# Kernel tuning notes

Hardware: AMD Instinct MI355X
Metric: run time of the kernel (lower is better)

## Reference

```python
import jax, jax.numpy as jnp
import numpy as np

# J2 (von Mises) plane-strain elastoplasticity with linear isotropic hardening
# (faithful stand-in for pyprnn's J2Material: elastic predictor + radial return,
#  committed history = plastic strain tensor + accumulated plastic strain).
E_MOD = 3130.0   # Young's modulus (epoxy, MPa)
NU = 0.37        # Poisson ratio
SIG_Y = 64.8     # initial yield stress
H_ISO = 300.0    # linear isotropic hardening modulus
MU = E_MOD / (2.0 * (1.0 + NU))
LAM = E_MOD * NU / ((1.0 + NU) * (1.0 - 2.0 * NU))


def j2_update(eps, eps_p, alpha):
    """eps: [P,3] (exx, eyy, gamma_xy engineering); eps_p: [P,4] (xx,yy,zz,xy tensorial);
    alpha: [P] accumulated plastic strain. Returns (stress [P,3], eps_p_new, alpha_new)."""
    ee_xx = eps[:, 0] - eps_p[:, 0]
    ee_yy = eps[:, 1] - eps_p[:, 1]
    ee_zz = -eps_p[:, 2]                      # plane strain: total ezz = 0
    ee_xy = 0.5 * eps[:, 2] - eps_p[:, 3]     # tensorial shear
    tr = ee_xx + ee_yy + ee_zz
    # trial (elastic predictor) stress
    sxx = LAM * tr + 2.0 * MU * ee_xx
    syy = LAM * tr + 2.0 * MU * ee_yy
    szz = LAM * tr + 2.0 * MU * ee_zz
    sxy = 2.0 * MU * ee_xy
    p = (sxx + syy + szz) / 3.0
    dxx, dyy, dzz = sxx - p, syy - p, szz - p
    q = jnp.sqrt(1.5 * (dxx * dxx + dyy * dyy + dzz * dzz + 2.0 * sxy * sxy))
    f = q - (SIG_Y + H_ISO * alpha)
    dgam = jnp.maximum(f, 0.0) / (3.0 * MU + H_ISO)   # radial return, closed form
    qs = jnp.maximum(q, 1e-12)
    nxx, nyy, nzz, nxy = 1.5 * dxx / qs, 1.5 * dyy / qs, 1.5 * dzz / qs, 1.5 * sxy / qs
    two_mu_dg = 2.0 * MU * dgam
    sig = jnp.stack([sxx - two_mu_dg * nxx, syy - two_mu_dg * nyy, sxy - two_mu_dg * nxy], axis=-1)
    eps_p_new = eps_p + dgam[:, None] * jnp.stack([nxx, nyy, nzz, nxy], axis=-1)
    alpha_new = alpha + dgam
    return sig, eps_p_new, alpha_new


def setup_inputs() -> dict:
    key = jax.random.key(0)
    k1, k2, k3 = jax.random.split(key, 3)
    B, T, F = 16384, 128, 3
    MATPTS = 16
    L, O = MATPTS * F, 3
    x = jax.random.normal(k1, (B, T, F), dtype=jnp.float32) * 0.02  # strain paths
    W1 = jax.random.normal(k2, (L, F), dtype=jnp.float32) * (1.0 / np.sqrt(F))
    W2 = jax.random.normal(k3, (O, L), dtype=jnp.float32) * (1.0 / np.sqrt(L))
    return {"x": x, "W1": W1, "W2": W2}


def reference(x, W1, W2):
    B, T, F = x.shape
    L = W1.shape[0]
    P = B * (L // F)                 # total material points = batch * mat_pts
    W2s = jax.nn.softplus(W2)        # SoftLayer: positive weights, no bias
    xt = jnp.swapaxes(x, 0, 1)       # [T, B, F]

    def step(carry, xi):
        eps_p, alpha = carry
        lat = xi @ W1.T                       # fc1 (no bias): [B, L]
        eps = lat.reshape(P, F)               # per-material-point strain
        sig, eps_p, alpha = j2_update(eps, eps_p, alpha)   # update + commit
        out = sig.reshape(B, L) @ W2s.T       # fc2 softplus-weighted linear
        return (eps_p, alpha), out

    carry0 = (jnp.zeros((P, 4), jnp.float32), jnp.zeros((P,), jnp.float32))
    _, ys = jax.lax.scan(step, carry0, xt)    # ys: [T, B, O]
    return jnp.swapaxes(ys, 0, 1)             # [B, T, O]
```

## Files before the change

kernel.cpp:

```cpp
#include <hip/hip_runtime.h>
#include <math.h>


#define BLOCK 256
#define BPB 32
#define TSTEPS 128
#define ROWF (TSTEPS * 3)

typedef float v2 __attribute__((ext_vector_type(2)));

static __device__ __forceinline__ v2 vfma(v2 a, v2 b, v2 c) {
    return __builtin_elementwise_fma(a, b, c);
}
static __device__ __forceinline__ v2 vmax(v2 a, v2 b) {
    return __builtin_elementwise_max(a, b);
}

#define DPP_ADDST(v, ctrl)                                                   \
    v += __int_as_float(__builtin_amdgcn_update_dpp(                         \
        0, __float_as_int(v), (ctrl), 0xf, 0xf, true))
#define RED8(v)                                                              \
    do { DPP_ADDST(v, 0xB1); DPP_ADDST(v, 0x4E); DPP_ADDST(v, 0x141); } while (0)

#define DPP_ST(r, ctrl) "v_add_f32_dpp %" #r ", %" #r ", %" #r " " ctrl \
                        " row_mask:0xf bank_mask:0xf\n\t"
#define DPP_STAGE(ctrl) \
    DPP_ST(0, ctrl) DPP_ST(1, ctrl) DPP_ST(2, ctrl)  DPP_ST(3, ctrl) \
    DPP_ST(4, ctrl) DPP_ST(5, ctrl) DPP_ST(6, ctrl)  DPP_ST(7, ctrl) \
    DPP_ST(8, ctrl) DPP_ST(9, ctrl) DPP_ST(10, ctrl) DPP_ST(11, ctrl)
#define DPP_BFLY12(a0,a1,a2,a3,a4,a5,a6,a7,a8,a9,a10,a11)                    \
  asm volatile(                                                              \
    "s_nop 1\n\t"                                                            \
    DPP_STAGE("quad_perm:[1,0,3,2]")                                         \
    DPP_STAGE("quad_perm:[2,3,0,1]")                                         \
    DPP_STAGE("row_half_mirror")                                             \
    : "+v"(a0), "+v"(a1), "+v"(a2), "+v"(a3), "+v"(a4), "+v"(a5),            \
      "+v"(a6), "+v"(a7), "+v"(a8), "+v"(a9), "+v"(a10), "+v"(a11))

__global__ __launch_bounds__(BLOCK, 2)
void prnn_j2_kernel(const float* __restrict__ x,
                    const float* __restrict__ W1,
                    const float* __restrict__ W2,
                    float* __restrict__ out)
{
    constexpr float MU    = (float)(3130.0 / (2.0 * (1.0 + 0.37)));
    constexpr float LAM   = (float)(3130.0 * 0.37 / ((1.0 + 0.37) * (1.0 - 2.0 * 0.37)));
    constexpr float SIG_Y = 64.8f;
    constexpr float H_ISO = 300.0f;
    const float TWO_MU  = 2.0f * MU;
    const float INV_DEN = 1.0f / (3.0f * MU + H_ISO);
    const float K3P     = (3.0f * MU) * INV_DEN;
    const float HP      = H_ISO * INV_DEN;
    const float CSC     = 1.0f / (MU * 2.4494897427831781f);
    const float Y0      = SIG_Y * CSC;

    const int tid = threadIdx.x;
    const int g   = tid >> 3;
    const int l   = tid & 7;
    const int gb  = blockIdx.x * BPB + g;

    const float* xb = x + gb * ROWF;
    float* ob = out + gb * ROWF;

    const int pa = l, pb = l + 8;
    v2 w1p[3][3], w2p[3][3];
    #pragma unroll
    for (int c = 0; c < 3; ++c)
        #pragma unroll
        for (int f = 0; f < 3; ++f) {
            float s = (c == 2) ? 0.5f : 1.0f;
            w1p[c][f].x = s * W1[(3 * pa + c) * 3 + f];
            w1p[c][f].y = s * W1[(3 * pb + c) * 3 + f];
        }
    #pragma unroll
    for (int o = 0; o < 3; ++o)
        #pragma unroll
        for (int c = 0; c < 3; ++c) {
            float wa = W2[o * 48 + 3 * pa + c];
            float wb = W2[o * 48 + 3 * pb + c];
            w2p[o][c].x = fmaxf(wa, 0.0f) + log1pf(expf(-fabsf(wa)));
            w2p[o][c].y = fmaxf(wb, 0.0f) + log1pf(expf(-fabsf(wb)));
        }

    float Mrow[3];
    {
        float Ms[3][3];
        #pragma unroll
        for (int f = 0; f < 3; ++f) {
            v2 ax = (LAM + TWO_MU) * w1p[0][f] + LAM * w1p[1][f];
            v2 ay = LAM * w1p[0][f] + (LAM + TWO_MU) * w1p[1][f];
            v2 as = TWO_MU * w1p[2][f];
            #pragma unroll
            for (int o = 0; o < 3; ++o) {
                v2 mp = vfma(w2p[o][0], ax, vfma(w2p[o][1], ay, w2p[o][2] * as));
                float ms = mp.x + mp.y;
                RED8(ms);
                Ms[o][f] = ms;
            }
        }
        #pragma unroll
        for (int f = 0; f < 3; ++f) {
            float v = (l == 0) ? Ms[0][f] : ((l == 1) ? Ms[1][f] : Ms[2][f]);
            Mrow[f] = v;
        }
    }

    v2 p0 = {0.f,0.f}, p1 = {0.f,0.f}, p2 = {0.f,0.f}, p3 = {0.f,0.f};
    v2 Y  = {Y0, Y0};
    v2 z0 = {0.f,0.f}, z1 = {0.f,0.f}, z2 = {0.f,0.f};

    const float4* xv = (const float4*)xb;
    const bool wact = (l < 3);
    float* obl = ob + l;

#define J2_PHYS(x0_, x1_, x2_, rr, mxv)                                      \
  {                                                                          \
    const float x0s = (x0_), x1s = (x1_), x2s = (x2_);                       \
    const v2 x0 = {x0s, x0s}, x1 = {x1s, x1s}, x2 = {x2s, x2s};              \
    const v2 wx0 = vfma(w1p[0][0], x0, vfma(w1p[0][1], x1, w1p[0][2] * x2)); \
    const v2 wx1 = vfma(w1p[1][0], x0, vfma(w1p[1][1], x1, w1p[1][2] * x2)); \
    const v2 wxy = vfma(w1p[2][0], x0, vfma(w1p[2][1], x1, w1p[2][2] * x2)); \
    const v2 c3  = (wx0 + wx1) * (1.0f / 3.0f);                              \
    const v2 ex0 = wx0 - c3;                                                 \
    const v2 ey0 = wx1 - c3;                                                 \
    const v2 exd = ex0 - p0;                                                 \
    const v2 eyd = ey0 - p1;                                                 \
    const v2 exy = wxy - p3;                                                 \
    const v2 szd = p2 + c3;                                      \
    const v2 t2 = exy * exy;                                                 \
    const v2 ua = vfma(eyd, eyd, exd * exd);                                 \
    const v2 ub = vfma(t2, (v2){2.0f, 2.0f}, szd * szd);                     \
    v2 u = ua + ub;                                                          \
    u = vmax(u, (v2){1e-30f, 1e-30f});                                       \
    v2 rq;                                                                   \
    rq.x = __builtin_amdgcn_rsqf(u.x);                                       \
    rq.y = __builtin_amdgcn_rsqf(u.y);                                       \
    const v2 su = u * rq;                                       \
    const v2 fY = vmax(su - Y, (v2){0.0f, 0.0f});                            \
    Y = vfma((v2){HP, HP}, fY, Y);                                           \
    const v2 k = (K3P * fY) * rq;                                            \
    const v2 kdx = k * exd;                                                  \
    const v2 kdy = k * eyd;                                                  \
    const v2 kdxy = k * exy;                                                 \
    p0 += kdx;                                                               \
    p1 += kdy;                                                               \
    p3 += kdxy;                                                              \
    p2 = p2 - k * szd;                                                       \
    z0 = vfma(w2p[0][0], kdx, vfma(w2p[0][1], kdy, vfma(w2p[0][2], kdxy, z0)));\
    z1 = vfma(w2p[1][0], kdx, vfma(w2p[1][1], kdy, vfma(w2p[1][2], kdxy, z1)));\
    z2 = vfma(w2p[2][0], kdx, vfma(w2p[2][1], kdy, vfma(w2p[2][2], kdxy, z2)));\
    (rr)[0] = z0.x + z0.y;                                                   \
    (rr)[1] = z1.x + z1.y;                                                   \
    (rr)[2] = z2.x + z2.y;                                                   \
    (mxv) = fmaf(Mrow[0], x0s, fmaf(Mrow[1], x1s, Mrow[2] * x2s));           \
  }

    float4 A0 = xv[0], A1 = xv[1], A2 = xv[2];

    for (int tb = 0; tb < TSTEPS / 4; ++tb) {
        const int nb = (tb < TSTEPS / 4 - 1) ? (3 * tb + 3) : (3 * tb);
        float4 An0 = xv[nb + 0];
        float4 An1 = xv[nb + 1];
        float4 An2 = xv[nb + 2];

        float r[12], mx[4];
        J2_PHYS(A0.x,  A0.y,  A0.z,  r + 0, mx[0]);
        J2_PHYS(A0.w,  A1.x,  A1.y,  r + 3, mx[1]);
        J2_PHYS(A1.z,  A1.w,  A2.x,  r + 6, mx[2]);
        J2_PHYS(A2.y,  A2.z,  A2.w,  r + 9, mx[3]);

        DPP_BFLY12(r[0], r[1], r[2], r[3], r[4], r[5],
                   r[6], r[7], r[8], r[9], r[10], r[11]);

        if (wact) {
            float zz0 = (l == 0) ? r[0] : ((l == 1) ? r[1]  : r[2]);
            float zz1 = (l == 0) ? r[3] : ((l == 1) ? r[4]  : r[5]);
            float zz2 = (l == 0) ? r[6] : ((l == 1) ? r[7]  : r[8]);
            float zz3 = (l == 0) ? r[9] : ((l == 1) ? r[10] : r[11]);
            obl[12 * tb + 0] = fmaf(-TWO_MU, zz0, mx[0]);
            obl[12 * tb + 3] = fmaf(-TWO_MU, zz1, mx[1]);
            obl[12 * tb + 6] = fmaf(-TWO_MU, zz2, mx[2]);
            obl[12 * tb + 9] = fmaf(-TWO_MU, zz3, mx[3]);
        }

        A0 = An0; A1 = An1; A2 = An2;
    }
#undef J2_PHYS
}

extern "C" void kernel_launch(void* const* d_in, const int* in_sizes, int n_in,
                              void* d_out, int out_size, void* d_ws, size_t ws_size,
                              hipStream_t stream) {
    const float* x  = (const float*)d_in[0];
    const float* W1 = (const float*)d_in[1];
    const float* W2 = (const float*)d_in[2];
    float* out = (float*)d_out;

    const int B = 16384;
    dim3 grid(B / BPB);
    dim3 block(BLOCK);
    prnn_j2_kernel<<<grid, block, 0, stream>>>(x, W1, W2, out);
}
```

Measured before the change: 118.7 us.

## Fold deviatoric projection into weights and process eight timesteps per iteration

Precomputes deviatoric-projected and sqrt2-scaled W1 rows so the per-step strain needs fewer ops, drops the separate zz plastic-strain state by using szd = exd+eyd, and rewrites the radial return with a single clamp on 1 - Y*rsqrt(u). It also doubles the time-step batch per loop iteration to 8, with a 24-register DPP butterfly and six float4 prefetches. Together these cut ALU work per step and amortize the reduction and store overhead, at the cost of higher register pressure under the 2-block launch bound.

```diff
diff --git a/kernel.cpp b/kernel.cpp
--- a/kernel.cpp
+++ b/kernel.cpp
@@ -24,18 +24,24 @@
 
 #define DPP_ST(r, ctrl) "v_add_f32_dpp %" #r ", %" #r ", %" #r " " ctrl \
                         " row_mask:0xf bank_mask:0xf\n\t"
-#define DPP_STAGE(ctrl) \
-    DPP_ST(0, ctrl) DPP_ST(1, ctrl) DPP_ST(2, ctrl)  DPP_ST(3, ctrl) \
-    DPP_ST(4, ctrl) DPP_ST(5, ctrl) DPP_ST(6, ctrl)  DPP_ST(7, ctrl) \
-    DPP_ST(8, ctrl) DPP_ST(9, ctrl) DPP_ST(10, ctrl) DPP_ST(11, ctrl)
-#define DPP_BFLY12(a0,a1,a2,a3,a4,a5,a6,a7,a8,a9,a10,a11)                    \
+#define DPP_STAGE24(ctrl) \
+    DPP_ST(0, ctrl)  DPP_ST(1, ctrl)  DPP_ST(2, ctrl)  DPP_ST(3, ctrl)  \
+    DPP_ST(4, ctrl)  DPP_ST(5, ctrl)  DPP_ST(6, ctrl)  DPP_ST(7, ctrl)  \
+    DPP_ST(8, ctrl)  DPP_ST(9, ctrl)  DPP_ST(10, ctrl) DPP_ST(11, ctrl) \
+    DPP_ST(12, ctrl) DPP_ST(13, ctrl) DPP_ST(14, ctrl) DPP_ST(15, ctrl) \
+    DPP_ST(16, ctrl) DPP_ST(17, ctrl) DPP_ST(18, ctrl) DPP_ST(19, ctrl) \
+    DPP_ST(20, ctrl) DPP_ST(21, ctrl) DPP_ST(22, ctrl) DPP_ST(23, ctrl)
+#define DPP_BFLY24(a0,a1,a2,a3,a4,a5,a6,a7,a8,a9,a10,a11,                    \
+                   a12,a13,a14,a15,a16,a17,a18,a19,a20,a21,a22,a23)          \
   asm volatile(                                                              \
     "s_nop 1\n\t"                                                            \
-    DPP_STAGE("quad_perm:[1,0,3,2]")                                         \
-    DPP_STAGE("quad_perm:[2,3,0,1]")                                         \
-    DPP_STAGE("row_half_mirror")                                             \
+    DPP_STAGE24("quad_perm:[1,0,3,2]")                                       \
+    DPP_STAGE24("quad_perm:[2,3,0,1]")                                       \
+    DPP_STAGE24("row_half_mirror")                                           \
     : "+v"(a0), "+v"(a1), "+v"(a2), "+v"(a3), "+v"(a4), "+v"(a5),            \
-      "+v"(a6), "+v"(a7), "+v"(a8), "+v"(a9), "+v"(a10), "+v"(a11))
+      "+v"(a6), "+v"(a7), "+v"(a8), "+v"(a9), "+v"(a10), "+v"(a11),          \
+      "+v"(a12), "+v"(a13), "+v"(a14), "+v"(a15), "+v"(a16), "+v"(a17),      \
+      "+v"(a18), "+v"(a19), "+v"(a20), "+v"(a21), "+v"(a22), "+v"(a23))
 
 __global__ __launch_bounds__(BLOCK, 2)
 void prnn_j2_kernel(const float* __restrict__ x,
@@ -53,6 +59,8 @@
     const float HP      = H_ISO * INV_DEN;
     const float CSC     = 1.0f / (MU * 2.4494897427831781f);
     const float Y0      = SIG_Y * CSC;
+    const float SQRT2   = 1.41421356237309515f;
+    const float RSQRT2  = 0.70710678118654752f;
 
     const int tid = threadIdx.x;
     const int g   = tid >> 3;
@@ -63,15 +71,17 @@
     float* ob = out + gb * ROWF;
 
     const int pa = l, pb = l + 8;
-    v2 w1p[3][3], w2p[3][3];
-    #pragma unroll
-    for (int c = 0; c < 3; ++c)
-        #pragma unroll
-        for (int f = 0; f < 3; ++f) {
-            float s = (c == 2) ? 0.5f : 1.0f;
-            w1p[c][f].x = s * W1[(3 * pa + c) * 3 + f];
-            w1p[c][f].y = s * W1[(3 * pb + c) * 3 + f];
-        }
+    v2 w1r0[3], w1r1[3], w1h2[3];
+    #pragma unroll
+    for (int f = 0; f < 3; ++f) {
+        w1r0[f].x = W1[(3 * pa + 0) * 3 + f];
+        w1r0[f].y = W1[(3 * pb + 0) * 3 + f];
+        w1r1[f].x = W1[(3 * pa + 1) * 3 + f];
+        w1r1[f].y = W1[(3 * pb + 1) * 3 + f];
+        w1h2[f].x = 0.5f * W1[(3 * pa + 2) * 3 + f];
+        w1h2[f].y = 0.5f * W1[(3 * pb + 2) * 3 + f];
+    }
+    v2 w2p[3][3];
     #pragma unroll
     for (int o = 0; o < 3; ++o)
         #pragma unroll
@@ -87,9 +97,9 @@
         float Ms[3][3];
         #pragma unroll
         for (int f = 0; f < 3; ++f) {
-            v2 ax = (LAM + TWO_MU) * w1p[0][f] + LAM * w1p[1][f];
-            v2 ay = LAM * w1p[0][f] + (LAM + TWO_MU) * w1p[1][f];
-            v2 as = TWO_MU * w1p[2][f];
+            v2 ax = (LAM + TWO_MU) * w1r0[f] + LAM * w1r1[f];
+            v2 ay = LAM * w1r0[f] + (LAM + TWO_MU) * w1r1[f];
+            v2 as = TWO_MU * w1h2[f];
             #pragma unroll
             for (int o = 0; o < 3; ++o) {
                 v2 mp = vfma(w2p[o][0], ax, vfma(w2p[o][1], ay, w2p[o][2] * as));
@@ -105,7 +115,17 @@
         }
     }
 
-    v2 p0 = {0.f,0.f}, p1 = {0.f,0.f}, p2 = {0.f,0.f}, p3 = {0.f,0.f};
+    v2 wdx[3], wdy[3], wsh[3];
+    #pragma unroll
+    for (int f = 0; f < 3; ++f) {
+        wdx[f] = (2.0f * w1r0[f] - w1r1[f]) * (1.0f / 3.0f);
+        wdy[f] = (2.0f * w1r1[f] - w1r0[f]) * (1.0f / 3.0f);
+        wsh[f] = SQRT2 * w1h2[f];
+    }
+    #pragma unroll
+    for (int o = 0; o < 3; ++o) w2p[o][2] *= RSQRT2;
+
+    v2 p0 = {0.f,0.f}, p1 = {0.f,0.f}, ps = {0.f,0.f};
     v2 Y  = {Y0, Y0};
     v2 z0 = {0.f,0.f}, z1 = {0.f,0.f}, z2 = {0.f,0.f};
 
@@ -117,38 +137,33 @@
   {                                                                          \
     const float x0s = (x0_), x1s = (x1_), x2s = (x2_);                       \
     const v2 x0 = {x0s, x0s}, x1 = {x1s, x1s}, x2 = {x2s, x2s};              \
-    const v2 wx0 = vfma(w1p[0][0], x0, vfma(w1p[0][1], x1, w1p[0][2] * x2)); \
-    const v2 wx1 = vfma(w1p[1][0], x0, vfma(w1p[1][1], x1, w1p[1][2] * x2)); \
-    const v2 wxy = vfma(w1p[2][0], x0, vfma(w1p[2][1], x1, w1p[2][2] * x2)); \
-    const v2 c3  = (wx0 + wx1) * (1.0f / 3.0f);                              \
-    const v2 ex0 = wx0 - c3;                                                 \
-    const v2 ey0 = wx1 - c3;                                                 \
+    const v2 ex0 = vfma(wdx[0], x0, vfma(wdx[1], x1, wdx[2] * x2));          \
+    const v2 ey0 = vfma(wdy[0], x0, vfma(wdy[1], x1, wdy[2] * x2));          \
+    const v2 wsy = vfma(wsh[0], x0, vfma(wsh[1], x1, wsh[2] * x2));          \
     const v2 exd = ex0 - p0;                                                 \
     const v2 eyd = ey0 - p1;                                                 \
-    const v2 exy = wxy - p3;                                                 \
-    const v2 szd = p2 + c3;                                      \
-    const v2 t2 = exy * exy;                                                 \
+    const v2 exy = wsy - ps;                                                 \
+    const v2 szd = exd + eyd;                             \
     const v2 ua = vfma(eyd, eyd, exd * exd);                                 \
-    const v2 ub = vfma(t2, (v2){2.0f, 2.0f}, szd * szd);                     \
+    const v2 ub = vfma(exy, exy, szd * szd);                                 \
     v2 u = ua + ub;                                                          \
     u = vmax(u, (v2){1e-30f, 1e-30f});                                       \
     v2 rq;                                                                   \
     rq.x = __builtin_amdgcn_rsqf(u.x);                                       \
     rq.y = __builtin_amdgcn_rsqf(u.y);                                       \
-    const v2 su = u * rq;                                       \
-    const v2 fY = vmax(su - Y, (v2){0.0f, 0.0f});                            \
-    Y = vfma((v2){HP, HP}, fY, Y);                                           \
-    const v2 k = (K3P * fY) * rq;                                            \
+    const v2 gm = vmax(vfma(-Y, rq, (v2){1.0f, 1.0f}), (v2){0.0f, 0.0f});    \
+    const v2 su = u * rq;                    \
+    const v2 k  = K3P * gm;                                                  \
+    Y = vfma((v2){HP, HP}, gm * su, Y);        \
     const v2 kdx = k * exd;                                                  \
     const v2 kdy = k * eyd;                                                  \
-    const v2 kdxy = k * exy;                                                 \
+    const v2 kdp = k * exy;                                                  \
     p0 += kdx;                                                               \
     p1 += kdy;                                                               \
-    p3 += kdxy;                                                              \
-    p2 = p2 - k * szd;                                                       \
-    z0 = vfma(w2p[0][0], kdx, vfma(w2p[0][1], kdy, vfma(w2p[0][2], kdxy, z0)));\
-    z1 = vfma(w2p[1][0], kdx, vfma(w2p[1][1], kdy, vfma(w2p[1][2], kdxy, z1)));\
-    z2 = vfma(w2p[2][0], kdx, vfma(w2p[2][1], kdy, vfma(w2p[2][2], kdxy, z2)));\
+    ps += kdp;                                                               \
+    z0 = vfma(w2p[0][0], kdx, vfma(w2p[0][1], kdy, vfma(w2p[0][2], kdp, z0)));\
+    z1 = vfma(w2p[1][0], kdx, vfma(w2p[1][1], kdy, vfma(w2p[1][2], kdp, z1)));\
+    z2 = vfma(w2p[2][0], kdx, vfma(w2p[2][1], kdy, vfma(w2p[2][2], kdp, z2)));\
     (rr)[0] = z0.x + z0.y;                                                   \
     (rr)[1] = z1.x + z1.y;                                                   \
     (rr)[2] = z2.x + z2.y;                                                   \
@@ -156,34 +171,42 @@
   }
 
     float4 A0 = xv[0], A1 = xv[1], A2 = xv[2];
-
-    for (int tb = 0; tb < TSTEPS / 4; ++tb) {
-        const int nb = (tb < TSTEPS / 4 - 1) ? (3 * tb + 3) : (3 * tb);
+    float4 A3 = xv[3], A4 = xv[4], A5 = xv[5];
+
+    for (int tb = 0; tb < TSTEPS / 8; ++tb) {
+        const int nb = (tb < TSTEPS / 8 - 1) ? (6 * tb + 6) : (6 * tb);
         float4 An0 = xv[nb + 0];
         float4 An1 = xv[nb + 1];
         float4 An2 = xv[nb + 2];
-
-        float r[12], mx[4];
-        J2_PHYS(A0.x,  A0.y,  A0.z,  r + 0, mx[0]);
-        J2_PHYS(A0.w,  A1.x,  A1.y,  r + 3, mx[1]);
-        J2_PHYS(A1.z,  A1.w,  A2.x,  r + 6, mx[2]);
-        J2_PHYS(A2.y,  A2.z,  A2.w,  r + 9, mx[3]);
-
-        DPP_BFLY12(r[0], r[1], r[2], r[3], r[4], r[5],
-                   r[6], r[7], r[8], r[9], r[10], r[11]);
+        float4 An3 = xv[nb + 3];
+        float4 An4 = xv[nb + 4];
+        float4 An5 = xv[nb + 5];
+
+        float r[24], mx[8];
+        J2_PHYS(A0.x, A0.y, A0.z, r + 0,  mx[0]);
+        J2_PHYS(A0.w, A1.x, A1.y, r + 3,  mx[1]);
+        J2_PHYS(A1.z, A1.w, A2.x, r + 6,  mx[2]);
+        J2_PHYS(A2.y, A2.z, A2.w, r + 9,  mx[3]);
+        J2_PHYS(A3.x, A3.y, A3.z, r + 12, mx[4]);
+        J2_PHYS(A3.w, A4.x, A4.y, r + 15, mx[5]);
+        J2_PHYS(A4.z, A4.w, A5.x, r + 18, mx[6]);
+        J2_PHYS(A5.y, A5.z, A5.w, r + 21, mx[7]);
+
+        DPP_BFLY24(r[0],  r[1],  r[2],  r[3],  r[4],  r[5],
+                   r[6],  r[7],  r[8],  r[9],  r[10], r[11],
+                   r[12], r[13], r[14], r[15], r[16], r[17],
+                   r[18], r[19], r[20], r[21], r[22], r[23]);
 
         if (wact) {
-            float zz0 = (l == 0) ? r[0] : ((l == 1) ? r[1]  : r[2]);
-            float zz1 = (l == 0) ? r[3] : ((l == 1) ? r[4]  : r[5]);
-            float zz2 = (l == 0) ? r[6] : ((l == 1) ? r[7]  : r[8]);
-            float zz3 = (l == 0) ? r[9] : ((l == 1) ? r[10] : r[11]);
-            obl[12 * tb + 0] = fmaf(-TWO_MU, zz0, mx[0]);
-            obl[12 * tb + 3] = fmaf(-TWO_MU, zz1, mx[1]);
-            obl[12 * tb + 6] = fmaf(-TWO_MU, zz2, mx[2]);
-            obl[12 * tb + 9] = fmaf(-TWO_MU, zz3, mx[3]);
+            #pragma unroll
+            for (int s = 0; s < 8; ++s) {
+                float zz = (l == 0) ? r[3*s] : ((l == 1) ? r[3*s+1] : r[3*s+2]);
+                obl[24 * tb + 3 * s] = fmaf(-TWO_MU, zz, mx[s]);
+            }
         }
 
         A0 = An0; A1 = An1; A2 = An2;
+        A3 = An3; A4 = An4; A5 = An5;
     }
 #undef J2_PHYS
 }
```

Measured after the change: 116.5 us. About the same (-1.9%).
